# Kernel tuning notes

Measured on AMD Instinct MI355X. Metric: run time of the kernel, lower is better.

The kernel has to match this reference:

```python
import jax, jax.numpy as jnp
import numpy as np


def setup_inputs() -> dict:
    key = jax.random.key(0)
    k1, k2, k3, k4 = jax.random.split(key, 4)
    B, S, TAGSET = 256, 256, 126
    T = TAGSET + 2  # includes START (T-2) and STOP (T-1)
    feats = jax.random.normal(k1, (B, S, T), dtype=jnp.float32)
    # gold tags only take real-tag values
    tags = jax.random.randint(k2, (B, S), 0, TAGSET).astype(jnp.int64)
    # prefix (length) mask, as required by length_mask = mask.sum(1)
    lengths = jax.random.randint(k3, (B,), S // 2, S + 1)
    mask = (jnp.arange(S)[None, :] < lengths[:, None]).astype(jnp.int32)
    # transitions param: matches init constraints of the module
    transitions = 0.1 * jax.random.normal(k4, (T, T), dtype=jnp.float32)
    transitions = transitions.at[:, T - 2].set(-1000.0)  # nothing -> START
    transitions = transitions.at[T - 1, :].set(-1000.0)  # STOP -> nothing
    return {"feats": feats, "transitions": transitions, "tags": tags, "mask": mask}


def _crf_nll(feats, transitions, tags, mask):
    B, S, T = feats.shape
    START, STOP = T - 2, T - 1
    feats_t = jnp.transpose(feats, (1, 0, 2))          # [S, B, T]
    mask_t = mask.T.astype(bool)                        # [S, B]

    # ---- log-partition (forward algorithm) ----
    # scores[t, b, i, j] = feats[t, b, j] + transitions[i, j]
    partition0 = feats_t[0] + transitions[START][None, :]  # [B, T]

    def step(partition, xs):
        feat, m = xs                                    # feat: [B, T], m: [B]
        # vals[b, i, j] = partition[b, i] + transitions[i, j] + feat[b, j]
        vals = partition[:, :, None] + transitions[None, :, :] + feat[:, None, :]
        new_p = jax.nn.logsumexp(vals, axis=1)          # [B, T]
        partition = jnp.where(m[:, None], new_p, partition)
        return partition, None

    partition, _ = jax.lax.scan(step, partition0, (feats_t[1:], mask_t[1:]))
    # final transition to STOP
    final_vals = partition[:, :, None] + transitions[None, :, :]  # [B, T, T]
    forward_score = jax.nn.logsumexp(final_vals, axis=1)[:, STOP].sum()

    # ---- gold path score ----
    prev = jnp.concatenate(
        [jnp.full((B, 1), START, dtype=tags.dtype), tags[:, :-1]], axis=1
    )                                                   # [B, S]
    emit = jnp.take_along_axis(feats, tags[:, :, None], axis=2)[:, :, 0]  # [B, S]
    trans = transitions[prev, tags]                     # [B, S]
    tg_energy = ((emit + trans) * mask.astype(feats.dtype)).sum()
    lengths = mask.sum(axis=1)                          # [B]
    end_ids = jnp.take_along_axis(tags, (lengths - 1)[:, None], axis=1)[:, 0]
    end_energy = transitions[end_ids, STOP].sum()
    gold_score = tg_energy + end_energy

    return forward_score - gold_score


def reference(feats, transitions, tags, mask):
    return _crf_nll(feats, transitions, tags, mask)
```

## Files before the change

### kernel.cpp

```cpp
#include <hip/hip_runtime.h>
#include <hip/hip_bf16.h>

#define B_ 256
#define S_ 256
#define T_ 128
#define START_ 126
#define STOP_ 127

typedef __attribute__((ext_vector_type(8))) short short8;
typedef __attribute__((ext_vector_type(4))) float f32x4;

__device__ __forceinline__ unsigned short f2bf(float f) {
    unsigned u = __float_as_uint(f);
    unsigned r = (u + 0x7FFFu + ((u >> 16) & 1u)) >> 16;
    return (unsigned short)r;
}

__device__ __forceinline__ float bf2f(unsigned short h) {
    return __uint_as_float(((unsigned)h) << 16);
}

__device__ __forceinline__ float red16max(float x) {
#if __has_builtin(__builtin_amdgcn_mov_dpp)
    x = fmaxf(x, __int_as_float(__builtin_amdgcn_mov_dpp(__float_as_int(x), 0x128, 0xF, 0xF, true)));
    x = fmaxf(x, __int_as_float(__builtin_amdgcn_mov_dpp(__float_as_int(x), 0x124, 0xF, 0xF, true)));
    x = fmaxf(x, __int_as_float(__builtin_amdgcn_mov_dpp(__float_as_int(x), 0x122, 0xF, 0xF, true)));
    x = fmaxf(x, __int_as_float(__builtin_amdgcn_mov_dpp(__float_as_int(x), 0x121, 0xF, 0xF, true)));
#else
    x = fmaxf(x, __shfl_xor(x, 8, 16));
    x = fmaxf(x, __shfl_xor(x, 4, 16));
    x = fmaxf(x, __shfl_xor(x, 2, 16));
    x = fmaxf(x, __shfl_xor(x, 1, 16));
#endif
    return x;
}

__device__ __forceinline__ float block_sum(float v, float* red, int tid) {
    #pragma unroll
    for (int o = 32; o; o >>= 1) v += __shfl_down(v, o, 64);
    __syncthreads();
    if ((tid & 63) == 0) red[tid >> 6] = v;
    __syncthreads();
    float r = (red[0] + red[1]) + (red[2] + red[3]);
    __syncthreads();
    return r;
}

__global__ __launch_bounds__(256) void crf_fwd(
    const float* __restrict__ feats,
    const float* __restrict__ trans,
    const int*   __restrict__ tags,
    const int*   __restrict__ mask,
    float* __restrict__ out)
{
    const int b    = blockIdx.x;
    const int tid  = threadIdx.x;
    const int lane = tid & 63;
    const int w    = tid >> 6;

    __shared__ __align__(16) unsigned short epb[2][T_];
    __shared__ float fbuf[2][8][T_];
    __shared__ float red[4];

    const float* fb_base = feats + (size_t)b * (S_ * T_);

    const int j0 = w * 32 + (lane & 15);
    const int j1 = j0 + 16;
    const int kg = (lane >> 4) * 8;

    short8 bfrag[4][2];
    {
        #pragma unroll
        for (int kt = 0; kt < 4; ++kt) {
            #pragma unroll
            for (int nt = 0; nt < 2; ++nt) {
                const int col = w * 32 + nt * 16 + (lane & 15);
                short8 f;
                #pragma unroll
                for (int r = 0; r < 8; ++r) {
                    const int k = kt * 32 + kg + r;
                    f[r] = (short)f2bf(__expf(trans[k * T_ + col]));
                }
                bfrag[kt][nt] = f;
            }
        }
    }

    {
        const int r = tid >> 5, c = (tid & 31) * 4;
        const float4 v = *(const float4*)&fb_base[tid * 4];
        float4 e;
        e.x = __expf(v.x); e.y = __expf(v.y); e.z = __expf(v.z); e.w = __expf(v.w);
        *(float4*)&fbuf[0][r][c] = e;
    }

    const int mk  = mask[b * S_ + tid];
    const int len = (int)(block_sum((float)mk, red, tid) + 0.5f);

    float M;

    {
        float u0 = fbuf[0][0][j0] * __expf(trans[START_ * T_ + j0]);
        float u1 = fbuf[0][0][j1] * __expf(trans[START_ * T_ + j1]);
        float m2 = red16max(fmaxf(u0, u1));
        if (lane == 0) red[w] = m2;
        __syncthreads();
        const float s  = fmaxf(fmaxf(red[0], red[1]), fmaxf(red[2], red[3]));
        const float rs = 1.0f / s;
        if (lane < 16) {
            epb[1][j0] = f2bf(u0 * rs);
            epb[1][j1] = f2bf(u1 * rs);
        }
        M = __logf(s);
        __syncthreads();
    }

    float4 pre = make_float4(0.f, 0.f, 0.f, 0.f);
    int pend = 0;
    for (int t = 1; t < len; ++t) {
        const int p  = t & 1;
        const int pn = p ^ 1;
        const int bc = (t >> 3) & 1;
        const int tr = t & 7;

        if (tr == 1) {
            const int nb = (t >> 3) + 1;
            if (nb < S_ / 8) {
                pre = *(const float4*)&fb_base[nb * (8 * T_) + tid * 4];
                pend = 1;
            }
        }

        const short8 a0 = *(const short8*)&epb[p][ 0 + kg];
        const short8 a1 = *(const short8*)&epb[p][32 + kg];
        const short8 a2 = *(const short8*)&epb[p][64 + kg];
        const short8 a3 = *(const short8*)&epb[p][96 + kg];

        f32x4 acc0 = {0.f, 0.f, 0.f, 0.f};
        f32x4 acc1 = {0.f, 0.f, 0.f, 0.f};
        acc0 = __builtin_amdgcn_mfma_f32_16x16x32_bf16(a0, bfrag[0][0], acc0, 0, 0, 0);
        acc0 = __builtin_amdgcn_mfma_f32_16x16x32_bf16(a1, bfrag[1][0], acc0, 0, 0, 0);
        acc0 = __builtin_amdgcn_mfma_f32_16x16x32_bf16(a2, bfrag[2][0], acc0, 0, 0, 0);
        acc0 = __builtin_amdgcn_mfma_f32_16x16x32_bf16(a3, bfrag[3][0], acc0, 0, 0, 0);
        acc1 = __builtin_amdgcn_mfma_f32_16x16x32_bf16(a0, bfrag[0][1], acc1, 0, 0, 0);
        acc1 = __builtin_amdgcn_mfma_f32_16x16x32_bf16(a1, bfrag[1][1], acc1, 0, 0, 0);
        acc1 = __builtin_amdgcn_mfma_f32_16x16x32_bf16(a2, bfrag[2][1], acc1, 0, 0, 0);
        acc1 = __builtin_amdgcn_mfma_f32_16x16x32_bf16(a3, bfrag[3][1], acc1, 0, 0, 0);

        float u0 = acc0[0] * fbuf[bc][tr][j0];
        float u1 = acc1[0] * fbuf[bc][tr][j1];

        if ((t & 3) == 0) {
            float m2 = red16max(fmaxf(u0, u1));
            if (lane == 0) red[w] = m2;
            __syncthreads();
            const float s  = fmaxf(fmaxf(red[0], red[1]), fmaxf(red[2], red[3]));
            const float rs = 1.0f / s;
            u0 *= rs; u1 *= rs;
            M += __logf(s);
        }

        if (lane < 16) {
            epb[pn][j0] = f2bf(u0);
            epb[pn][j1] = f2bf(u1);
        }

        if (tr == 7 && pend) {
            const int nb = (t >> 3) + 1;
            const int r = tid >> 5, c = (tid & 31) * 4;
            float4 e;
            e.x = __expf(pre.x); e.y = __expf(pre.y);
            e.z = __expf(pre.z); e.w = __expf(pre.w);
            *(float4*)&fbuf[nb & 1][r][c] = e;
            pend = 0;
        }

        __syncthreads();
    }

    const int pf = len & 1;
    float v = 0.f;
    if (tid < T_) {
        v = bf2f(epb[pf][tid]) * __expf(trans[tid * T_ + STOP_]);
    }
    const float ssum = block_sum(v, red, tid);
    const float fwd  = M + __logf(ssum);

    const int tg = tags[b * S_ + tid];
    float g = 0.f;
    if (mk) {
        const int prev = (tid == 0) ? START_ : tags[b * S_ + tid - 1];
        g = fb_base[tid * T_ + tg] + trans[prev * T_ + tg];
    }
    if (tid == len - 1) g += trans[tg * T_ + STOP_];
    const float gold = block_sum(g, red, tid);

    if (tid == 0) atomicAdd(out, fwd - gold);
}

extern "C" void kernel_launch(void* const* d_in, const int* in_sizes, int n_in,
                              void* d_out, int out_size, void* d_ws, size_t ws_size,
                              hipStream_t stream) {
    const float* feats = (const float*)d_in[0];
    const float* trans = (const float*)d_in[1];
    const int*   tags  = (const int*)d_in[2];
    const int*   mask  = (const int*)d_in[3];
    float* out = (float*)d_out;

    hipMemsetAsync(out, 0, sizeof(float), stream);

    crf_fwd<<<dim3(B_), dim3(256), 0, stream>>>(feats, trans, tags, mask, out);
}
```

Before: 159.0 us.

## Run CRF forward recurrence in a single wavefront with register-resident state

Each sequence now runs on one 64-lane wavefront instead of four, holding the whole exp(transitions) B-fragment set in registers. The partition vector is passed between steps with ds_bpermute instead of LDS plus __syncthreads. Feats are prefetched per 8-step block into registers. Rescaling uses lane 0's value rather than a block max. This removes the per-step barriers and shared-memory round trips that sit on the serial dependency chain. In exchange each wave issues 4x more MFMAs per step, uses far more registers, and the cheaper normalisation may risk precision or overflow.

```diff
diff --git a/kernel.cpp b/kernel.cpp
--- a/kernel.cpp
+++ b/kernel.cpp
@@ -9,6 +9,7 @@
 
 typedef __attribute__((ext_vector_type(8))) short short8;
 typedef __attribute__((ext_vector_type(4))) float f32x4;
+typedef __attribute__((ext_vector_type(4))) int i32x4;
 
 __device__ __forceinline__ unsigned short f2bf(float f) {
     unsigned u = __float_as_uint(f);
@@ -16,186 +17,134 @@
     return (unsigned short)r;
 }
 
-__device__ __forceinline__ float bf2f(unsigned short h) {
-    return __uint_as_float(((unsigned)h) << 16);
-}
-
-__device__ __forceinline__ float red16max(float x) {
-#if __has_builtin(__builtin_amdgcn_mov_dpp)
-    x = fmaxf(x, __int_as_float(__builtin_amdgcn_mov_dpp(__float_as_int(x), 0x128, 0xF, 0xF, true)));
-    x = fmaxf(x, __int_as_float(__builtin_amdgcn_mov_dpp(__float_as_int(x), 0x124, 0xF, 0xF, true)));
-    x = fmaxf(x, __int_as_float(__builtin_amdgcn_mov_dpp(__float_as_int(x), 0x122, 0xF, 0xF, true)));
-    x = fmaxf(x, __int_as_float(__builtin_amdgcn_mov_dpp(__float_as_int(x), 0x121, 0xF, 0xF, true)));
-#else
-    x = fmaxf(x, __shfl_xor(x, 8, 16));
-    x = fmaxf(x, __shfl_xor(x, 4, 16));
-    x = fmaxf(x, __shfl_xor(x, 2, 16));
-    x = fmaxf(x, __shfl_xor(x, 1, 16));
-#endif
-    return x;
-}
-
-__device__ __forceinline__ float block_sum(float v, float* red, int tid) {
-    #pragma unroll
-    for (int o = 32; o; o >>= 1) v += __shfl_down(v, o, 64);
-    __syncthreads();
-    if ((tid & 63) == 0) red[tid >> 6] = v;
-    __syncthreads();
-    float r = (red[0] + red[1]) + (red[2] + red[3]);
-    __syncthreads();
-    return r;
-}
-
-__global__ __launch_bounds__(256) void crf_fwd(
+__global__ __launch_bounds__(64, 1) void crf_fwd(
     const float* __restrict__ feats,
     const float* __restrict__ trans,
     const int*   __restrict__ tags,
     const int*   __restrict__ mask,
     float* __restrict__ out)
 {
-    const int b    = blockIdx.x;
-    const int tid  = threadIdx.x;
-    const int lane = tid & 63;
-    const int w    = tid >> 6;
+    const int b = blockIdx.x;
+    const int l = threadIdx.x;
+    const int g = l >> 4;
+    const int c = l & 15;
 
-    __shared__ __align__(16) unsigned short epb[2][T_];
-    __shared__ float fbuf[2][8][T_];
-    __shared__ float red[4];
+    const float* fb = feats + (size_t)b * (S_ * T_);
 
-    const float* fb_base = feats + (size_t)b * (S_ * T_);
-
-    const int j0 = w * 32 + (lane & 15);
-    const int j1 = j0 + 16;
-    const int kg = (lane >> 4) * 8;
-
-    short8 bfrag[4][2];
-    {
+    short8 bfrag[4][8];
+    #pragma unroll
+    for (int kt = 0; kt < 4; ++kt) {
         #pragma unroll
-        for (int kt = 0; kt < 4; ++kt) {
+        for (int nt = 0; nt < 8; ++nt) {
+            short8 f;
             #pragma unroll
-            for (int nt = 0; nt < 2; ++nt) {
-                const int col = w * 32 + nt * 16 + (lane & 15);
-                short8 f;
-                #pragma unroll
-                for (int r = 0; r < 8; ++r) {
-                    const int k = kt * 32 + kg + r;
-                    f[r] = (short)f2bf(__expf(trans[k * T_ + col]));
-                }
-                bfrag[kt][nt] = f;
+            for (int e = 0; e < 8; ++e) {
+                const int k = kt * 16 + 4 * g + (e >> 1) + 64 * (e & 1);
+                f[e] = (short)f2bf(__expf(trans[k * T_ + nt * 16 + c]));
             }
+            bfrag[kt][nt] = f;
         }
     }
 
-    {
-        const int r = tid >> 5, c = (tid & 31) * 4;
-        const float4 v = *(const float4*)&fb_base[tid * 4];
-        float4 e;
-        e.x = __expf(v.x); e.y = __expf(v.y); e.z = __expf(v.z); e.w = __expf(v.w);
-        *(float4*)&fbuf[0][r][c] = e;
+    int cnt = 0;
+    #pragma unroll
+    for (int s4 = 0; s4 < 4; ++s4) cnt += mask[b * S_ + s4 * 64 + l];
+    #pragma unroll
+    for (int o = 32; o; o >>= 1) cnt += __shfl_xor(cnt, o, 64);
+    const int len = cnt;
+
+    float cf[16], nf[16];
+    #pragma unroll
+    for (int r = 0; r < 8; ++r) {
+        cf[2 * r]     = fb[r * T_ + l];
+        cf[2 * r + 1] = fb[r * T_ + 64 + l];
     }
 
-    const int mk  = mask[b * S_ + tid];
-    const int len = (int)(block_sum((float)mk, red, tid) + 0.5f);
+    float u0 = __expf(cf[0] + trans[START_ * T_ + l]);
+    float u1 = __expf(cf[1] + trans[START_ * T_ + 64 + l]);
+    float M = 0.f;
 
-    float M;
-
-    {
-        float u0 = fbuf[0][0][j0] * __expf(trans[START_ * T_ + j0]);
-        float u1 = fbuf[0][0][j1] * __expf(trans[START_ * T_ + j1]);
-        float m2 = red16max(fmaxf(u0, u1));
-        if (lane == 0) red[w] = m2;
-        __syncthreads();
-        const float s  = fmaxf(fmaxf(red[0], red[1]), fmaxf(red[2], red[3]));
-        const float rs = 1.0f / s;
-        if (lane < 16) {
-            epb[1][j0] = f2bf(u0 * rs);
-            epb[1][j1] = f2bf(u1 * rs);
-        }
-        M = __logf(s);
-        __syncthreads();
-    }
-
-    float4 pre = make_float4(0.f, 0.f, 0.f, 0.f);
-    int pend = 0;
-    for (int t = 1; t < len; ++t) {
-        const int p  = t & 1;
-        const int pn = p ^ 1;
-        const int bc = (t >> 3) & 1;
-        const int tr = t & 7;
-
-        if (tr == 1) {
-            const int nb = (t >> 3) + 1;
-            if (nb < S_ / 8) {
-                pre = *(const float4*)&fb_base[nb * (8 * T_) + tid * 4];
-                pend = 1;
+    for (int blk = 0; blk < 32; ++blk) {
+        if (blk + 1 < 32) {
+            #pragma unroll
+            for (int r = 0; r < 8; ++r) {
+                nf[2 * r]     = fb[((blk + 1) * 8 + r) * T_ + l];
+                nf[2 * r + 1] = fb[((blk + 1) * 8 + r) * T_ + 64 + l];
             }
         }
+        #pragma unroll
+        for (int r = 0; r < 8; ++r) {
+            const int tt = blk * 8 + r;
+            if (r == 0 && blk == 0) continue;
+            if (tt >= len) goto done;
+            {
+                unsigned pk;
+                asm("v_cvt_pk_bf16_f32 %0, %1, %2" : "=v"(pk) : "v"(u0), "v"(u1));
+                i32x4 w[4];
+                #pragma unroll
+                for (int kt = 0; kt < 4; ++kt) {
+                    #pragma unroll
+                    for (int q = 0; q < 4; ++q) {
+                        w[kt][q] = __builtin_amdgcn_ds_bpermute(
+                            64 * kt + 16 * g + 4 * q, (int)pk);
+                    }
+                }
+                f32x4 acc[8];
+                #pragma unroll
+                for (int n = 0; n < 8; ++n) acc[n] = (f32x4){0.f, 0.f, 0.f, 0.f};
+                #pragma unroll
+                for (int kt = 0; kt < 4; ++kt) {
+                    const short8 a = *(const short8*)&w[kt];
+                    #pragma unroll
+                    for (int n = 0; n < 8; ++n)
+                        acc[n] = __builtin_amdgcn_mfma_f32_16x16x32_bf16(
+                            a, bfrag[kt][n], acc[n], 0, 0, 0);
+                }
+                float lo0 = (g & 1) ? acc[1][0] : acc[0][0];
+                float hi0 = (g & 1) ? acc[3][0] : acc[2][0];
+                float v0  = (g & 2) ? hi0 : lo0;
+                float lo1 = (g & 1) ? acc[5][0] : acc[4][0];
+                float hi1 = (g & 1) ? acc[7][0] : acc[6][0];
+                float v1  = (g & 2) ? hi1 : lo1;
+                u0 = v0 * __expf(cf[2 * r]);
+                u1 = v1 * __expf(cf[2 * r + 1]);
+                if ((tt & 3) == 0) {
+                    const float sc = __shfl(u0, 0, 64);
+                    const float rs = 1.0f / sc;
+                    u0 *= rs;
+                    u1 *= rs;
+                    M += __logf(sc);
+                }
+            }
+        }
+        if (blk + 1 < 32) {
+            #pragma unroll
+            for (int i = 0; i < 16; ++i) cf[i] = nf[i];
+        }
+    }
+done: ;
 
-        const short8 a0 = *(const short8*)&epb[p][ 0 + kg];
-        const short8 a1 = *(const short8*)&epb[p][32 + kg];
-        const short8 a2 = *(const short8*)&epb[p][64 + kg];
-        const short8 a3 = *(const short8*)&epb[p][96 + kg];
+    float v = u0 * __expf(trans[l * T_ + STOP_])
+            + u1 * __expf(trans[(64 + l) * T_ + STOP_]);
+    #pragma unroll
+    for (int o = 32; o; o >>= 1) v += __shfl_xor(v, o, 64);
+    const float fwd = M + __logf(v);
 
-        f32x4 acc0 = {0.f, 0.f, 0.f, 0.f};
-        f32x4 acc1 = {0.f, 0.f, 0.f, 0.f};
-        acc0 = __builtin_amdgcn_mfma_f32_16x16x32_bf16(a0, bfrag[0][0], acc0, 0, 0, 0);
-        acc0 = __builtin_amdgcn_mfma_f32_16x16x32_bf16(a1, bfrag[1][0], acc0, 0, 0, 0);
-        acc0 = __builtin_amdgcn_mfma_f32_16x16x32_bf16(a2, bfrag[2][0], acc0, 0, 0, 0);
-        acc0 = __builtin_amdgcn_mfma_f32_16x16x32_bf16(a3, bfrag[3][0], acc0, 0, 0, 0);
-        acc1 = __builtin_amdgcn_mfma_f32_16x16x32_bf16(a0, bfrag[0][1], acc1, 0, 0, 0);
-        acc1 = __builtin_amdgcn_mfma_f32_16x16x32_bf16(a1, bfrag[1][1], acc1, 0, 0, 0);
-        acc1 = __builtin_amdgcn_mfma_f32_16x16x32_bf16(a2, bfrag[2][1], acc1, 0, 0, 0);
-        acc1 = __builtin_amdgcn_mfma_f32_16x16x32_bf16(a3, bfrag[3][1], acc1, 0, 0, 0);
+    float gg = 0.f;
+    #pragma unroll
+    for (int s4 = 0; s4 < 4; ++s4) {
+        const int s = s4 * 64 + l;
+        if (mask[b * S_ + s]) {
+            const int tg = tags[b * S_ + s];
+            const int pv = (s == 0) ? START_ : tags[b * S_ + s - 1];
+            gg += fb[s * T_ + tg] + trans[pv * T_ + tg];
+            if (s == len - 1) gg += trans[tg * T_ + STOP_];
+        }
+    }
+    #pragma unroll
+    for (int o = 32; o; o >>= 1) gg += __shfl_xor(gg, o, 64);
 
-        float u0 = acc0[0] * fbuf[bc][tr][j0];
-        float u1 = acc1[0] * fbuf[bc][tr][j1];
-
-        if ((t & 3) == 0) {
-            float m2 = red16max(fmaxf(u0, u1));
-            if (lane == 0) red[w] = m2;
-            __syncthreads();
-            const float s  = fmaxf(fmaxf(red[0], red[1]), fmaxf(red[2], red[3]));
-            const float rs = 1.0f / s;
-            u0 *= rs; u1 *= rs;
-            M += __logf(s);
-        }
-
-        if (lane < 16) {
-            epb[pn][j0] = f2bf(u0);
-            epb[pn][j1] = f2bf(u1);
-        }
-
-        if (tr == 7 && pend) {
-            const int nb = (t >> 3) + 1;
-            const int r = tid >> 5, c = (tid & 31) * 4;
-            float4 e;
-            e.x = __expf(pre.x); e.y = __expf(pre.y);
-            e.z = __expf(pre.z); e.w = __expf(pre.w);
-            *(float4*)&fbuf[nb & 1][r][c] = e;
-            pend = 0;
-        }
-
-        __syncthreads();
-    }
-
-    const int pf = len & 1;
-    float v = 0.f;
-    if (tid < T_) {
-        v = bf2f(epb[pf][tid]) * __expf(trans[tid * T_ + STOP_]);
-    }
-    const float ssum = block_sum(v, red, tid);
-    const float fwd  = M + __logf(ssum);
-
-    const int tg = tags[b * S_ + tid];
-    float g = 0.f;
-    if (mk) {
-        const int prev = (tid == 0) ? START_ : tags[b * S_ + tid - 1];
-        g = fb_base[tid * T_ + tg] + trans[prev * T_ + tg];
-    }
-    if (tid == len - 1) g += trans[tg * T_ + STOP_];
-    const float gold = block_sum(g, red, tid);
-
-    if (tid == 0) atomicAdd(out, fwd - gold);
+    if (l == 0) atomicAdd(out, fwd - gg);
 }
 
 extern "C" void kernel_launch(void* const* d_in, const int* in_sizes, int n_in,
@@ -208,6 +157,5 @@
     float* out = (float*)d_out;
 
     hipMemsetAsync(out, 0, sizeof(float), stream);
-
-    crf_fwd<<<dim3(B_), dim3(256), 0, stream>>>(feats, trans, tags, mask, out);
+    crf_fwd<<<dim3(B_), dim3(64), 0, stream>>>(feats, trans, tags, mask, out);
 }
```

Measured after the change: 191.6 us. +20.4%, slower.
